# Kernel optimization log

Hardware: AMD Instinct MI355X
Metric: run time of the kernel (lower is better)

## Reference

```python
import jax, jax.numpy as jnp
import numpy as np

EPS_LN1 = 1e-6   # partial(nn.LayerNorm, eps=1e-6)
EPS_OUT = 1e-5   # nn.LayerNorm default inside SS3D out_norm


def _layernorm(x, w, b, eps):
    m = jnp.mean(x, axis=-1, keepdims=True)
    v = jnp.var(x, axis=-1, keepdims=True)
    return (x - m) * jax.lax.rsqrt(v + eps) * w + b


def _selective_scan(dA, dBx):
    # dA, dBx: (B, K, d, L, N); linear recurrence h_t = dA_t * h_{t-1} + dBx_t
    def comb(c1, c2):
        a1, b1 = c1
        a2, b2 = c2
        return a2 * a1, a2 * b1 + b2
    _, hs = jax.lax.associative_scan(comb, (dA, dBx), axis=3)
    return hs  # (B, K, d, L, N)


def setup_inputs() -> dict:
    key = jax.random.key(0)
    ks = jax.random.split(key, 12)
    B, D, H, W, C = 1, 16, 16, 16, 96
    d, N, K, R = 96, 16, 6, 6  # d_inner, d_state, n_scan_dirs, dt_rank
    s = 0.02
    f = lambda k, shp: jax.random.normal(k, shp, dtype=jnp.float32)
    return {
        "x": f(ks[0], (B, D, H, W, C)),
        "ln1_w": jnp.ones((C,), jnp.float32),
        "ln1_b": jnp.zeros((C,), jnp.float32),
        "in_proj_w": f(ks[1], (2 * d, C)) * s,
        "conv_w": f(ks[2], (d, 1, 3, 3, 3)) * s,
        "conv_b": f(ks[3], (d,)) * s,
        "x_proj_w": f(ks[4], (K, R + 2 * N, d)) * s,
        "dt_proj_w": f(ks[5], (K, d, R)) * s,
        "dt_proj_b": f(ks[6], (K, d)) * s,
        "A_log": jnp.log(1.0 + 15.0 * jax.random.uniform(ks[7], (K, d, N), jnp.float32)),
        "D_skip": f(ks[8], (K, d)) * s,
        "out_norm_w": jnp.ones((d,), jnp.float32),
        "out_norm_b": jnp.zeros((d,), jnp.float32),
        "out_proj_w": f(ks[9], (C, d)) * s,
    }


def reference(x, ln1_w, ln1_b, in_proj_w, conv_w, conv_b, x_proj_w,
              dt_proj_w, dt_proj_b, A_log, D_skip, out_norm_w, out_norm_b,
              out_proj_w):
    B, D, H, W, C = x.shape
    L = D * H * W
    K, _, d = x_proj_w.shape
    R = dt_proj_w.shape[2]
    N = A_log.shape[2]

    # pre-norm
    xn = _layernorm(x, ln1_w, ln1_b, EPS_LN1)

    # in_proj -> (x, z)
    xz = jnp.einsum('bdhwc,ec->bdhwe', xn, in_proj_w)  # (B,D,H,W,2d)
    xh, z = jnp.split(xz, 2, axis=-1)

    # depthwise 3x3x3 conv + SiLU, channels-first
    xc = jnp.transpose(xh, (0, 4, 1, 2, 3))  # (B,d,D,H,W)
    xc = jax.lax.conv_general_dilated(
        xc, conv_w, window_strides=(1, 1, 1), padding='SAME',
        dimension_numbers=('NCDHW', 'OIDHW', 'NCDHW'),
        feature_group_count=d)
    xc = jax.nn.silu(xc + conv_b[None, :, None, None, None])

    # K = 6 scan orderings: DHW, HWD, WDH and their reverses
    o0 = xc.reshape(B, d, L)
    o1 = jnp.transpose(xc, (0, 1, 3, 4, 2)).reshape(B, d, L)  # (H,W,D) order
    o2 = jnp.transpose(xc, (0, 1, 4, 2, 3)).reshape(B, d, L)  # (W,D,H) order
    fwd3 = jnp.stack([o0, o1, o2], axis=1)                    # (B,3,d,L)
    xs = jnp.concatenate([fwd3, jnp.flip(fwd3, axis=-1)], axis=1)  # (B,K,d,L)

    # per-direction input-dependent parameters
    x_dbl = jnp.einsum('bkdl,kcd->bkcl', xs, x_proj_w)        # (B,K,R+2N,L)
    dt, Bm, Cm = jnp.split(x_dbl, [R, R + N], axis=2)
    dts = jnp.einsum('bkrl,kdr->bkdl', dt, dt_proj_w) + dt_proj_b[None, :, :, None]
    dts = jax.nn.softplus(dts)                                # delta_softplus

    A = -jnp.exp(A_log)                                       # (K,d,N)
    dA = jnp.exp(dts[..., None] * A[None, :, :, None, :])     # (B,K,d,L,N)
    Bt = jnp.transpose(Bm, (0, 1, 3, 2))                      # (B,K,L,N)
    dBx = (dts * xs)[..., None] * Bt[:, :, None, :, :]        # (B,K,d,L,N)

    hs = _selective_scan(dA, dBx)                             # (B,K,d,L,N)
    Ct = jnp.transpose(Cm, (0, 1, 3, 2))                      # (B,K,L,N)
    ys = jnp.einsum('bkdln,bkln->bkdl', hs, Ct) + D_skip[None, :, :, None] * xs

    # undo reversals and orderings, sum the 6 paths
    yf = ys[:, :3] + jnp.flip(ys[:, 3:], axis=-1)             # (B,3,d,L)
    y0 = yf[:, 0]
    y1 = jnp.transpose(yf[:, 1].reshape(B, d, H, W, D), (0, 1, 4, 2, 3)).reshape(B, d, L)
    y2 = jnp.transpose(yf[:, 2].reshape(B, d, W, D, H), (0, 1, 3, 4, 2)).reshape(B, d, L)
    y = (y0 + y1 + y2).reshape(B, d, D, H, W)
    y = jnp.transpose(y, (0, 2, 3, 4, 1))                     # (B,D,H,W,d)

    # out_norm, gate, out_proj
    y = _layernorm(y, out_norm_w, out_norm_b, EPS_OUT)
    y = y * jax.nn.silu(z)
    out = jnp.einsum('bdhwe,ce->bdhwc', y, out_proj_w)

    # residual (drop_path is identity at eval)
    return x + out
```

## Files before the change

### kernel.cpp

```cpp
#include <hip/hip_runtime.h>
#include <hip/hip_bf16.h>

#define L 4096
#define CDIM 96
#define DDIM 96
#define KDIR 6
#define NST 16
#define RRK 6
#define YH 32
#define NCHUNK 256
#define CHLEN 16

typedef _Float16 half4v __attribute__((ext_vector_type(4)));

__device__ __forceinline__ float sigmoidf_(float x) { return 1.f / (1.f + __expf(-x)); }

__device__ __forceinline__ int sigma_k(int kb, int l) {
    if (kb == 0) return l;
    if (kb == 1) return ((l & 15) << 8) | ((l >> 8) << 4) | ((l >> 4) & 15);
    return (((l >> 4) & 15) << 8) | ((l & 15) << 4) | (l >> 8);
}

__global__ void __launch_bounds__(192) k1_ln_inproj(
        const float* __restrict__ x, const float* __restrict__ ln_w,
        const float* __restrict__ ln_b, const float* __restrict__ Wp,
        _Float16* __restrict__ xhh, _Float16* __restrict__ zsh) {
    int s0 = blockIdx.x * 8;
    int tid = threadIdx.x;
    __shared__ __align__(16) float xt[8][96];
    __shared__ __align__(16) float xn[8][96];
    __shared__ float mss[8], rss[8];
    ((float4*)&xt[0][0])[tid] = ((const float4*)(x + (size_t)s0 * 96))[tid];
    __syncthreads();
    int wave = tid >> 6, lane = tid & 63;
    for (int r = wave; r < 8; r += 3) {
        float v = xt[r][lane] + ((lane < 32) ? xt[r][64 + lane] : 0.f);
#pragma unroll
        for (int off = 1; off < 64; off <<= 1) v += __shfl_xor(v, off);
        float vs = xt[r][lane] * xt[r][lane] + ((lane < 32) ? xt[r][64 + lane] * xt[r][64 + lane] : 0.f);
#pragma unroll
        for (int off = 1; off < 64; off <<= 1) vs += __shfl_xor(vs, off);
        if (lane == 0) {
            float mean = v * (1.f / 96.f);
            float var = vs * (1.f / 96.f) - mean * mean;
            mss[r] = mean; rss[r] = rsqrtf(var + 1e-6f);
        }
    }
    __syncthreads();
    {
        int r = tid / 24, c4 = tid % 24;
        float4 xv = ((float4*)&xt[r][0])[c4];
        float4 wv = ((const float4*)ln_w)[c4];
        float4 bv = ((const float4*)ln_b)[c4];
        float m = mss[r], rs = rss[r];
        float4 o;
        o.x = (xv.x - m) * rs * wv.x + bv.x;
        o.y = (xv.y - m) * rs * wv.y + bv.y;
        o.z = (xv.z - m) * rs * wv.z + bv.z;
        o.w = (xv.w - m) * rs * wv.w + bv.w;
        ((float4*)&xn[r][0])[c4] = o;
    }
    float4 Wr[24];
    const float4* wr = (const float4*)(Wp + (size_t)tid * 96);
#pragma unroll
    for (int c4 = 0; c4 < 24; c4++) Wr[c4] = wr[c4];
    __syncthreads();
#pragma unroll
    for (int s = 0; s < 8; s++) {
        const float4* xr4 = (const float4*)&xn[s][0];
        float a0 = 0.f, a1 = 0.f, a2 = 0.f, a3 = 0.f;
#pragma unroll
        for (int c4 = 0; c4 < 24; c4 += 4) {
            float4 x0 = xr4[c4], x1 = xr4[c4 + 1], x2 = xr4[c4 + 2], x3 = xr4[c4 + 3];
            a0 += Wr[c4].x * x0.x + Wr[c4].y * x0.y + Wr[c4].z * x0.z + Wr[c4].w * x0.w;
            a1 += Wr[c4+1].x * x1.x + Wr[c4+1].y * x1.y + Wr[c4+1].z * x1.z + Wr[c4+1].w * x1.w;
            a2 += Wr[c4+2].x * x2.x + Wr[c4+2].y * x2.y + Wr[c4+2].z * x2.z + Wr[c4+2].w * x2.w;
            a3 += Wr[c4+3].x * x3.x + Wr[c4+3].y * x3.y + Wr[c4+3].z * x3.z + Wr[c4+3].w * x3.w;
        }
        float acc = (a0 + a1) + (a2 + a3);
        if (tid < 96) xhh[(size_t)tid * L + s0 + s] = (_Float16)acc;
        else zsh[(size_t)(s0 + s) * 96 + (tid - 96)] = (_Float16)(acc * sigmoidf_(acc));
    }
}

__global__ void k2_conv(const _Float16* __restrict__ xhh, const float* __restrict__ cw,
                        const float* __restrict__ cb, _Float16* __restrict__ xch,
                        _Float16* __restrict__ xcTh) {
    int idx = blockIdx.x * 256 + threadIdx.x;
    int c = idx >> 12, s = idx & 4095;
    int dz = s >> 8, h = (s >> 4) & 15, w = s & 15;
    const _Float16* xin = xhh + (size_t)c * L;
    const float* wc = cw + c * 27;
    float acc = cb[c];
#pragma unroll
    for (int i = 0; i < 3; i++) {
        int z2 = dz + i - 1; if ((unsigned)z2 > 15u) continue;
#pragma unroll
        for (int j = 0; j < 3; j++) {
            int h2 = h + j - 1; if ((unsigned)h2 > 15u) continue;
#pragma unroll
            for (int kk = 0; kk < 3; kk++) {
                int w2 = w + kk - 1; if ((unsigned)w2 > 15u) continue;
                acc += (float)xin[z2 * 256 + h2 * 16 + w2] * wc[i * 9 + j * 3 + kk];
            }
        }
    }
    float r = acc * sigmoidf_(acc);
    _Float16 hr = (_Float16)r;
    xch[(size_t)c * L + s] = hr;
    xcTh[(size_t)s * 96 + c] = hr;
}

__global__ void k3_xproj(const _Float16* __restrict__ xch, const float* __restrict__ Wx,
                         const float* __restrict__ Wdt, const float* __restrict__ bdt,
                         _Float16* __restrict__ Y2h, _Float16* __restrict__ Zsh) {
    int k = blockIdx.x;
    int tid = threadIdx.x;
    int sbase = blockIdx.y * 256;
    int s = sbase + tid;
    int g = blockIdx.z;
    __shared__ float dts[256][6];
    float acc[14];
#pragma unroll
    for (int i = 0; i < 14; i++) acc[i] = 0.f;
    const float* wdt_rows = Wx + (size_t)k * 38 * DDIM;
    const float* wbc      = Wx + ((size_t)k * 38 + 6 + g * 8) * DDIM;
    for (int dd = 0; dd < 96; dd += 4) {
        float v[4];
#pragma unroll
        for (int j = 0; j < 4; j++) v[j] = (float)xch[(size_t)(dd + j) * L + s];
#pragma unroll
        for (int j = 0; j < 4; j++) {
#pragma unroll
            for (int r = 0; r < 6; r++) acc[r] += wdt_rows[r * DDIM + dd + j] * v[j];
#pragma unroll
            for (int i = 0; i < 8; i++) acc[6 + i] += wbc[i * DDIM + dd + j] * v[j];
        }
    }
    _Float16* yo = Y2h + ((size_t)k * L + s) * YH;
#pragma unroll
    for (int i = 0; i < 8; i++) yo[g * 8 + i] = (_Float16)acc[6 + i];
#pragma unroll
    for (int r = 0; r < 6; r++) dts[tid][r] = acc[r];
    __syncthreads();
    for (int i = 0; i < 24; i++) {
        int idx = i * 256 + tid;
        int dl = idx % 24;
        int sr = idx / 24;
        int d = g * 24 + dl;
        const float* wr = Wdt + ((size_t)k * 96 + d) * 6;
        float a = bdt[k * 96 + d];
#pragma unroll
        for (int r = 0; r < 6; r++) a += wr[r] * dts[sr][r];
        float sp = (a > 15.f) ? a : __logf(1.f + __expf(a));
        Zsh[((size_t)k * L + sbase + sr) * 96 + d] = (_Float16)sp;
    }
}


__global__ void __launch_bounds__(256) ka_scan(
        const _Float16* __restrict__ Zsh, const _Float16* __restrict__ xcTh,
        const _Float16* __restrict__ Y2h, const float* __restrict__ A_log,
        _Float16* __restrict__ Aah, _Float16* __restrict__ Abh) {
    int t = blockIdx.x * 256 + threadIdx.x;
    int nq = t & 3;
    int q = t >> 2;
    int d = q % 96;
    int rest = q / 96;
    int chunk = rest % NCHUNK;
    int k = rest / NCHUNK;
    int kb = (k < 3) ? k : (k - 3);
    bool flip = (k >= 3);
    float An[4];
    {
        float4 al = *(const float4*)(A_log + ((size_t)k * 96 + d) * 16 + nq * 4);
        An[0] = -__expf(al.x); An[1] = -__expf(al.y);
        An[2] = -__expf(al.z); An[3] = -__expf(al.w);
    }
    float a[4] = {1.f, 1.f, 1.f, 1.f};
    float b[4] = {0.f, 0.f, 0.f, 0.f};
    const _Float16* Zk = Zsh + (size_t)k * L * 96;
    const _Float16* Yk = Y2h + (size_t)k * L * YH;
    int l0 = chunk * CHLEN;
    for (int i = 0; i < CHLEN; i += 4) {
        int sI[4]; float dt[4], xv[4]; half4v Bh[4];
#pragma unroll
        for (int j = 0; j < 4; j++) {
            int l = l0 + i + j;
            int lp = flip ? (4095 - l) : l;
            sI[j] = sigma_k(kb, lp);
        }
#pragma unroll
        for (int j = 0; j < 4; j++) {
            dt[j] = (float)Zk[(size_t)sI[j] * 96 + d];
            xv[j] = (float)xcTh[(size_t)sI[j] * 96 + d];
            Bh[j] = *(const half4v*)(Yk + (size_t)sI[j] * YH + nq * 4);
        }
#pragma unroll
        for (int j = 0; j < 4; j++) {
            float dtx = dt[j] * xv[j];
            float e0 = __expf(dt[j] * An[0]);
            float e1 = __expf(dt[j] * An[1]);
            float e2 = __expf(dt[j] * An[2]);
            float e3 = __expf(dt[j] * An[3]);
            b[0] = e0 * b[0] + dtx * (float)Bh[j].x; a[0] *= e0;
            b[1] = e1 * b[1] + dtx * (float)Bh[j].y; a[1] *= e1;
            b[2] = e2 * b[2] + dtx * (float)Bh[j].z; a[2] *= e2;
            b[3] = e3 * b[3] + dtx * (float)Bh[j].w; a[3] *= e3;
        }
    }
    size_t o = (((size_t)k * NCHUNK + chunk) * 96 + d) * 16 + nq * 4;
    half4v ha, hb;
    ha.x = (_Float16)a[0]; ha.y = (_Float16)a[1]; ha.z = (_Float16)a[2]; ha.w = (_Float16)a[3];
    hb.x = (_Float16)b[0]; hb.y = (_Float16)b[1]; hb.z = (_Float16)b[2]; hb.w = (_Float16)b[3];
    *(half4v*)(Aah + o) = ha;
    *(half4v*)(Abh + o) = hb;
}

__global__ void __launch_bounds__(256) kb_combine(
        const _Float16* __restrict__ Aah, const _Float16* __restrict__ Abh,
        _Float16* __restrict__ Pbh) {
    int t = blockIdx.x * 256 + threadIdx.x;
    int n = t & 15;
    int rest = t >> 4;
    int d = rest % 96;
    int k = rest / 96;
    size_t base = ((size_t)k * NCHUNK * 96 + d) * 16 + n;
    const size_t cstride = 96 * 16;
    float rb = 0.f;
    for (int c0 = 0; c0 < NCHUNK; c0 += 16) {
        float av[16], bv[16];
#pragma unroll
        for (int j = 0; j < 16; j++) {
            av[j] = (float)Aah[base + (size_t)(c0 + j) * cstride];
            bv[j] = (float)Abh[base + (size_t)(c0 + j) * cstride];
        }
#pragma unroll
        for (int j = 0; j < 16; j++) {
            Pbh[base + (size_t)(c0 + j) * cstride] = (_Float16)rb;
            rb = av[j] * rb + bv[j];
        }
    }
}

__global__ void __launch_bounds__(256) kc_apply(
        const _Float16* __restrict__ Zsh, const _Float16* __restrict__ xcTh,
        const _Float16* __restrict__ Y2h, const float* __restrict__ A_log,
        const float* __restrict__ D_skip, const _Float16* __restrict__ Pbh,
        _Float16* __restrict__ ysh) {
    int t = blockIdx.x * 256 + threadIdx.x;
    int nq = t & 3;
    int q = t >> 2;
    int d = q % 96;
    int rest = q / 96;
    int chunk = rest % NCHUNK;
    int k = rest / NCHUNK;
    int kb = (k < 3) ? k : (k - 3);
    bool flip = (k >= 3);
    float An[4];
    {
        float4 al = *(const float4*)(A_log + ((size_t)k * 96 + d) * 16 + nq * 4);
        An[0] = -__expf(al.x); An[1] = -__expf(al.y);
        An[2] = -__expf(al.z); An[3] = -__expf(al.w);
    }
    float Dk = D_skip[k * DDIM + d];
    float h[4];
    {
        half4v hp = *(const half4v*)(Pbh + (((size_t)k * NCHUNK + chunk) * 96 + d) * 16 + nq * 4);
        h[0] = (float)hp.x; h[1] = (float)hp.y; h[2] = (float)hp.z; h[3] = (float)hp.w;
    }
    const _Float16* Zk = Zsh + (size_t)k * L * 96;
    const _Float16* Yk = Y2h + (size_t)k * L * YH;
    int l0 = chunk * CHLEN;
    for (int i = 0; i < CHLEN; i += 4) {
        int sI[4]; float dt[4], xv[4]; half4v Bh[4], Ch[4];
#pragma unroll
        for (int j = 0; j < 4; j++) {
            int l = l0 + i + j;
            int lp = flip ? (4095 - l) : l;
            sI[j] = sigma_k(kb, lp);
        }
#pragma unroll
        for (int j = 0; j < 4; j++) {
            dt[j] = (float)Zk[(size_t)sI[j] * 96 + d];
            xv[j] = (float)xcTh[(size_t)sI[j] * 96 + d];
            Bh[j] = *(const half4v*)(Yk + (size_t)sI[j] * YH + nq * 4);
            Ch[j] = *(const half4v*)(Yk + (size_t)sI[j] * YH + 16 + nq * 4);
        }
#pragma unroll
        for (int j = 0; j < 4; j++) {
            float dtx = dt[j] * xv[j];
            float e0 = __expf(dt[j] * An[0]);
            float e1 = __expf(dt[j] * An[1]);
            float e2 = __expf(dt[j] * An[2]);
            float e3 = __expf(dt[j] * An[3]);
            h[0] = e0 * h[0] + dtx * (float)Bh[j].x;
            h[1] = e1 * h[1] + dtx * (float)Bh[j].y;
            h[2] = e2 * h[2] + dtx * (float)Bh[j].z;
            h[3] = e3 * h[3] + dtx * (float)Bh[j].w;
            float p = h[0] * (float)Ch[j].x + h[1] * (float)Ch[j].y
                    + h[2] * (float)Ch[j].z + h[3] * (float)Ch[j].w;
            p += __shfl_xor(p, 1);
            p += __shfl_xor(p, 2);
            if (nq == 0) ysh[((size_t)sI[j] * KDIR + k) * 96 + d] = (_Float16)(p + Dk * xv[j]);
        }
    }
}

__global__ void __launch_bounds__(192) k6_out(
        const _Float16* __restrict__ ysh, const _Float16* __restrict__ zsh,
        const float* __restrict__ onw, const float* __restrict__ onb,
        const float* __restrict__ Wo, const float* __restrict__ x,
        float* __restrict__ out) {
    int s0 = blockIdx.x * 8;
    int tid = threadIdx.x;
    __shared__ __align__(16) float vt[8][96];
    __shared__ __align__(16) float gt[8][96];
    __shared__ float mss[8], rss[8];
#pragma unroll
    for (int j = 0; j < 4; j++) {
        int f = tid + j * 192;
        int sr = f / 96, c = f % 96;
        const _Float16* yr = ysh + ((size_t)(s0 + sr) * KDIR) * 96 + c;
        float v = 0.f;
#pragma unroll
        for (int k = 0; k < KDIR; k++) v += (float)yr[k * 96];
        vt[sr][c] = v;
    }
    __syncthreads();
    int wave = tid >> 6, lane = tid & 63;
    for (int r = wave; r < 8; r += 3) {
        float v = vt[r][lane] + ((lane < 32) ? vt[r][64 + lane] : 0.f);
#pragma unroll
        for (int off = 1; off < 64; off <<= 1) v += __shfl_xor(v, off);
        float vs = vt[r][lane] * vt[r][lane] + ((lane < 32) ? vt[r][64 + lane] * vt[r][64 + lane] : 0.f);
#pragma unroll
        for (int off = 1; off < 64; off <<= 1) vs += __shfl_xor(vs, off);
        if (lane == 0) {
            float mean = v * (1.f / 96.f);
            float var = vs * (1.f / 96.f) - mean * mean;
            mss[r] = mean; rss[r] = rsqrtf(var + 1e-5f);
        }
    }
    __syncthreads();
#pragma unroll
    for (int j = 0; j < 4; j++) {
        int f = tid + j * 192;
        int sr = f / 96, c = f % 96;
        float g = (vt[sr][c] - mss[sr]) * rss[sr] * onw[c] + onb[c];
        gt[sr][c] = g * (float)zsh[(size_t)(s0 + sr) * 96 + c];
    }
    int e = tid % 96, sg = tid / 96;
    float4 Wr[24];
    const float4* wr = (const float4*)(Wo + (size_t)e * 96);
#pragma unroll
    for (int c4 = 0; c4 < 24; c4++) Wr[c4] = wr[c4];
    __syncthreads();
#pragma unroll
    for (int j = 0; j < 4; j++) {
        int s = sg * 4 + j;
        const float4* g4 = (const float4*)&gt[s][0];
        float a0 = 0.f, a1 = 0.f, a2 = 0.f, a3 = 0.f;
#pragma unroll
        for (int c4 = 0; c4 < 24; c4 += 4) {
            float4 x0 = g4[c4], x1 = g4[c4 + 1], x2 = g4[c4 + 2], x3 = g4[c4 + 3];
            a0 += Wr[c4].x * x0.x + Wr[c4].y * x0.y + Wr[c4].z * x0.z + Wr[c4].w * x0.w;
            a1 += Wr[c4+1].x * x1.x + Wr[c4+1].y * x1.y + Wr[c4+1].z * x1.z + Wr[c4+1].w * x1.w;
            a2 += Wr[c4+2].x * x2.x + Wr[c4+2].y * x2.y + Wr[c4+2].z * x2.z + Wr[c4+2].w * x2.w;
            a3 += Wr[c4+3].x * x3.x + Wr[c4+3].y * x3.y + Wr[c4+3].z * x3.z + Wr[c4+3].w * x3.w;
        }
        float acc = (a0 + a1) + (a2 + a3) + x[(size_t)(s0 + s) * 96 + e];
        out[(size_t)(s0 + s) * 96 + e] = acc;
    }
}

extern "C" void kernel_launch(void* const* d_in, const int* in_sizes, int n_in,
                              void* d_out, int out_size, void* d_ws, size_t ws_size,
                              hipStream_t stream) {
    const float* x        = (const float*)d_in[0];
    const float* ln1_w    = (const float*)d_in[1];
    const float* ln1_b    = (const float*)d_in[2];
    const float* in_proj  = (const float*)d_in[3];
    const float* conv_w   = (const float*)d_in[4];
    const float* conv_b   = (const float*)d_in[5];
    const float* x_proj   = (const float*)d_in[6];
    const float* dt_w     = (const float*)d_in[7];
    const float* dt_b     = (const float*)d_in[8];
    const float* A_log    = (const float*)d_in[9];
    const float* D_skip   = (const float*)d_in[10];
    const float* onw      = (const float*)d_in[11];
    const float* onb      = (const float*)d_in[12];
    const float* out_w    = (const float*)d_in[13];
    float* out = (float*)d_out;

    _Float16* xhh  = (_Float16*)d_ws;
    _Float16* zsh  = xhh + (size_t)96 * L;
    _Float16* xch  = zsh + (size_t)96 * L;
    _Float16* xcTh = xch + (size_t)96 * L;
    _Float16* Y2h  = xcTh + (size_t)96 * L;
    _Float16* Zsh  = Y2h + (size_t)KDIR * L * YH;
    _Float16* ysh  = Zsh + (size_t)KDIR * L * 96;
    _Float16* Aah  = ysh + (size_t)L * KDIR * 96;
    _Float16* Abh  = Aah + (size_t)KDIR * NCHUNK * DDIM * NST;
    _Float16* Pbh  = Abh + (size_t)KDIR * NCHUNK * DDIM * NST;

    k1_ln_inproj<<<dim3(L / 8), dim3(192), 0, stream>>>(x, ln1_w, ln1_b, in_proj, xhh, zsh);
    k2_conv<<<dim3(96 * L / 256), dim3(256), 0, stream>>>(xhh, conv_w, conv_b, xch, xcTh);
    k3_xproj<<<dim3(KDIR, 16, 4), dim3(256), 0, stream>>>(xch, x_proj, dt_w, dt_b, Y2h, Zsh);
    ka_scan<<<dim3(KDIR * NCHUNK * DDIM * 4 / 256), dim3(256), 0, stream>>>(Zsh, xcTh, Y2h, A_log, Aah, Abh);
    kb_combine<<<dim3(KDIR * DDIM * NST / 256), dim3(256), 0, stream>>>(Aah, Abh, Pbh);
    kc_apply<<<dim3(KDIR * NCHUNK * DDIM * 4 / 256), dim3(256), 0, stream>>>(Zsh, xcTh, Y2h, A_log, D_skip, Pbh, ysh);
    k6_out<<<dim3(L / 8), dim3(192), 0, stream>>>(ysh, zsh, onw, onb, out_w, x, out);
}
```

Baseline: 178.7 us.

## Fuse all seven stages into one cooperative persistent kernel with grid syncs

Replaces the seven separate kernel launches with a single cooperative kernel of 512 persistent blocks. Each stage runs as a grid-stride loop and is separated from the next by grid.sync(). The aim is to remove launch overhead and inter-kernel gaps. In exchange, some stages lose per-stage tuned block shapes: 192-thread stages now run in 256-thread blocks with threads idle. Grid barriers also add their own cost. If the cooperative launch fails, it falls back to the original launches.

After: 531.4 us. 197% more time.

```diff
diff --git a/kernel.cpp b/kernel.cpp
--- a/kernel.cpp
+++ b/kernel.cpp
@@ -1,5 +1,8 @@
 #include <hip/hip_runtime.h>
 #include <hip/hip_bf16.h>
+#include <hip/hip_cooperative_groups.h>
+
+namespace cg = cooperative_groups;
 
 #define L 4096
 #define CDIM 96
@@ -10,6 +13,7 @@
 #define YH 32
 #define NCHUNK 256
 #define CHLEN 16
+#define GRIDN 512
 
 typedef _Float16 half4v __attribute__((ext_vector_type(4)));
 
@@ -20,6 +24,374 @@
     if (kb == 1) return ((l & 15) << 8) | ((l >> 8) << 4) | ((l >> 4) & 15);
     return (((l >> 4) & 15) << 8) | ((l & 15) << 4) | (l >> 8);
 }
+
+__global__ void __launch_bounds__(256, 2) fused_vss(
+        const float* __restrict__ x, const float* __restrict__ ln1_w,
+        const float* __restrict__ ln1_b, const float* __restrict__ in_proj,
+        const float* __restrict__ conv_w, const float* __restrict__ conv_b,
+        const float* __restrict__ x_proj, const float* __restrict__ dt_w,
+        const float* __restrict__ dt_b, const float* __restrict__ A_log,
+        const float* __restrict__ D_skip, const float* __restrict__ onw,
+        const float* __restrict__ onb, const float* __restrict__ out_w,
+        float* __restrict__ out,
+        _Float16* __restrict__ xhh, _Float16* __restrict__ zsh,
+        _Float16* __restrict__ xch, _Float16* __restrict__ xcTh,
+        _Float16* __restrict__ Y2h, _Float16* __restrict__ Zsh,
+        _Float16* __restrict__ ysh, _Float16* __restrict__ Aah,
+        _Float16* __restrict__ Abh, _Float16* __restrict__ Pbh) {
+    cg::grid_group grid = cg::this_grid();
+    const int tid = threadIdx.x;
+    const int bid = blockIdx.x;
+    const int G = gridDim.x;
+
+    __shared__ __align__(16) float smA[8][96];
+    __shared__ __align__(16) float smB[8][96];
+    __shared__ float sms[8], smr[8];
+    __shared__ float dts[256][6];
+
+    for (int u = bid; u < L / 8; u += G) {
+        int s0 = u * 8;
+        if (tid < 192)
+            ((float4*)&smA[0][0])[tid] = ((const float4*)(x + (size_t)s0 * 96))[tid];
+        __syncthreads();
+        int wave = tid >> 6, lane = tid & 63;
+        for (int r = wave; r < 8; r += 4) {
+            float v = smA[r][lane] + ((lane < 32) ? smA[r][64 + lane] : 0.f);
+#pragma unroll
+            for (int off = 1; off < 64; off <<= 1) v += __shfl_xor(v, off);
+            float vs = smA[r][lane] * smA[r][lane] + ((lane < 32) ? smA[r][64 + lane] * smA[r][64 + lane] : 0.f);
+#pragma unroll
+            for (int off = 1; off < 64; off <<= 1) vs += __shfl_xor(vs, off);
+            if (lane == 0) {
+                float mean = v * (1.f / 96.f);
+                float var = vs * (1.f / 96.f) - mean * mean;
+                sms[r] = mean; smr[r] = rsqrtf(var + 1e-6f);
+            }
+        }
+        __syncthreads();
+        if (tid < 192) {
+            int r = tid / 24, c4 = tid % 24;
+            float4 xv = ((float4*)&smA[r][0])[c4];
+            float4 wv = ((const float4*)ln1_w)[c4];
+            float4 bv = ((const float4*)ln1_b)[c4];
+            float m = sms[r], rs = smr[r];
+            float4 o;
+            o.x = (xv.x - m) * rs * wv.x + bv.x;
+            o.y = (xv.y - m) * rs * wv.y + bv.y;
+            o.z = (xv.z - m) * rs * wv.z + bv.z;
+            o.w = (xv.w - m) * rs * wv.w + bv.w;
+            ((float4*)&smB[r][0])[c4] = o;
+        }
+        float4 Wr[24];
+        if (tid < 192) {
+            const float4* wr = (const float4*)(in_proj + (size_t)tid * 96);
+#pragma unroll
+            for (int c4 = 0; c4 < 24; c4++) Wr[c4] = wr[c4];
+        }
+        __syncthreads();
+        if (tid < 192) {
+#pragma unroll
+            for (int s = 0; s < 8; s++) {
+                const float4* xr4 = (const float4*)&smB[s][0];
+                float a0 = 0.f, a1 = 0.f, a2 = 0.f, a3 = 0.f;
+#pragma unroll
+                for (int c4 = 0; c4 < 24; c4 += 4) {
+                    float4 x0 = xr4[c4], x1 = xr4[c4 + 1], x2 = xr4[c4 + 2], x3 = xr4[c4 + 3];
+                    a0 += Wr[c4].x * x0.x + Wr[c4].y * x0.y + Wr[c4].z * x0.z + Wr[c4].w * x0.w;
+                    a1 += Wr[c4+1].x * x1.x + Wr[c4+1].y * x1.y + Wr[c4+1].z * x1.z + Wr[c4+1].w * x1.w;
+                    a2 += Wr[c4+2].x * x2.x + Wr[c4+2].y * x2.y + Wr[c4+2].z * x2.z + Wr[c4+2].w * x2.w;
+                    a3 += Wr[c4+3].x * x3.x + Wr[c4+3].y * x3.y + Wr[c4+3].z * x3.z + Wr[c4+3].w * x3.w;
+                }
+                float acc = (a0 + a1) + (a2 + a3);
+                if (tid < 96) xhh[(size_t)tid * L + s0 + s] = (_Float16)acc;
+                else zsh[(size_t)(s0 + s) * 96 + (tid - 96)] = (_Float16)(acc * sigmoidf_(acc));
+            }
+        }
+        __syncthreads();
+    }
+    grid.sync();
+
+    for (int u = bid; u < (96 * L) / 256; u += G) {
+        int idx = u * 256 + tid;
+        int c = idx >> 12, s = idx & 4095;
+        int dz = s >> 8, h = (s >> 4) & 15, w = s & 15;
+        const _Float16* xin = xhh + (size_t)c * L;
+        const float* wc = conv_w + c * 27;
+        float acc = conv_b[c];
+#pragma unroll
+        for (int i = 0; i < 3; i++) {
+            int z2 = dz + i - 1; if ((unsigned)z2 > 15u) continue;
+#pragma unroll
+            for (int j = 0; j < 3; j++) {
+                int h2 = h + j - 1; if ((unsigned)h2 > 15u) continue;
+#pragma unroll
+                for (int kk = 0; kk < 3; kk++) {
+                    int w2 = w + kk - 1; if ((unsigned)w2 > 15u) continue;
+                    acc += (float)xin[z2 * 256 + h2 * 16 + w2] * wc[i * 9 + j * 3 + kk];
+                }
+            }
+        }
+        float r = acc * sigmoidf_(acc);
+        _Float16 hr = (_Float16)r;
+        xch[(size_t)c * L + s] = hr;
+        xcTh[(size_t)s * 96 + c] = hr;
+    }
+    grid.sync();
+
+    for (int u = bid; u < 384; u += G) {
+        int k = u % 6;
+        int sb = (u / 6) % 16;
+        int g = u / 96;
+        int sbase = sb * 256;
+        int s = sbase + tid;
+        float acc[14];
+#pragma unroll
+        for (int i = 0; i < 14; i++) acc[i] = 0.f;
+        const float* wdt_rows = x_proj + (size_t)k * 38 * DDIM;
+        const float* wbc      = x_proj + ((size_t)k * 38 + 6 + g * 8) * DDIM;
+        for (int dd = 0; dd < 96; dd += 4) {
+            float v[4];
+#pragma unroll
+            for (int j = 0; j < 4; j++) v[j] = (float)xch[(size_t)(dd + j) * L + s];
+#pragma unroll
+            for (int j = 0; j < 4; j++) {
+#pragma unroll
+                for (int r = 0; r < 6; r++) acc[r] += wdt_rows[r * DDIM + dd + j] * v[j];
+#pragma unroll
+                for (int i = 0; i < 8; i++) acc[6 + i] += wbc[i * DDIM + dd + j] * v[j];
+            }
+        }
+        _Float16* yo = Y2h + ((size_t)k * L + s) * YH;
+#pragma unroll
+        for (int i = 0; i < 8; i++) yo[g * 8 + i] = (_Float16)acc[6 + i];
+#pragma unroll
+        for (int r = 0; r < 6; r++) dts[tid][r] = acc[r];
+        __syncthreads();
+        for (int i = 0; i < 24; i++) {
+            int idx = i * 256 + tid;
+            int dl = idx % 24;
+            int sr = idx / 24;
+            int d = g * 24 + dl;
+            const float* wr = dt_w + ((size_t)k * 96 + d) * 6;
+            float a = dt_b[k * 96 + d];
+#pragma unroll
+            for (int r = 0; r < 6; r++) a += wr[r] * dts[sr][r];
+            float sp = (a > 15.f) ? a : __logf(1.f + __expf(a));
+            Zsh[((size_t)k * L + sbase + sr) * 96 + d] = (_Float16)sp;
+        }
+        __syncthreads();
+    }
+    grid.sync();
+
+    for (int u = bid; u < KDIR * NCHUNK * DDIM * 4 / 256; u += G) {
+        int t = u * 256 + tid;
+        int nq = t & 3;
+        int q = t >> 2;
+        int d = q % 96;
+        int rest = q / 96;
+        int chunk = rest % NCHUNK;
+        int k = rest / NCHUNK;
+        int kb = (k < 3) ? k : (k - 3);
+        bool flip = (k >= 3);
+        float An[4];
+        {
+            float4 al = *(const float4*)(A_log + ((size_t)k * 96 + d) * 16 + nq * 4);
+            An[0] = -__expf(al.x); An[1] = -__expf(al.y);
+            An[2] = -__expf(al.z); An[3] = -__expf(al.w);
+        }
+        float a[4] = {1.f, 1.f, 1.f, 1.f};
+        float b[4] = {0.f, 0.f, 0.f, 0.f};
+        const _Float16* Zk = Zsh + (size_t)k * L * 96;
+        const _Float16* Yk = Y2h + (size_t)k * L * YH;
+        int l0 = chunk * CHLEN;
+        for (int i = 0; i < CHLEN; i += 4) {
+            int sI[4]; float dt[4], xv[4]; half4v Bh[4];
+#pragma unroll
+            for (int j = 0; j < 4; j++) {
+                int l = l0 + i + j;
+                int lp = flip ? (4095 - l) : l;
+                sI[j] = sigma_k(kb, lp);
+            }
+#pragma unroll
+            for (int j = 0; j < 4; j++) {
+                dt[j] = (float)Zk[(size_t)sI[j] * 96 + d];
+                xv[j] = (float)xcTh[(size_t)sI[j] * 96 + d];
+                Bh[j] = *(const half4v*)(Yk + (size_t)sI[j] * YH + nq * 4);
+            }
+#pragma unroll
+            for (int j = 0; j < 4; j++) {
+                float dtx = dt[j] * xv[j];
+                float e0 = __expf(dt[j] * An[0]);
+                float e1 = __expf(dt[j] * An[1]);
+                float e2 = __expf(dt[j] * An[2]);
+                float e3 = __expf(dt[j] * An[3]);
+                b[0] = e0 * b[0] + dtx * (float)Bh[j].x; a[0] *= e0;
+                b[1] = e1 * b[1] + dtx * (float)Bh[j].y; a[1] *= e1;
+                b[2] = e2 * b[2] + dtx * (float)Bh[j].z; a[2] *= e2;
+                b[3] = e3 * b[3] + dtx * (float)Bh[j].w; a[3] *= e3;
+            }
+        }
+        size_t o = (((size_t)k * NCHUNK + chunk) * 96 + d) * 16 + nq * 4;
+        half4v ha, hb;
+        ha.x = (_Float16)a[0]; ha.y = (_Float16)a[1]; ha.z = (_Float16)a[2]; ha.w = (_Float16)a[3];
+        hb.x = (_Float16)b[0]; hb.y = (_Float16)b[1]; hb.z = (_Float16)b[2]; hb.w = (_Float16)b[3];
+        *(half4v*)(Aah + o) = ha;
+        *(half4v*)(Abh + o) = hb;
+    }
+    grid.sync();
+
+    for (int u = bid; u < KDIR * DDIM * NST / 256; u += G) {
+        int t = u * 256 + tid;
+        int n = t & 15;
+        int rest = t >> 4;
+        int d = rest % 96;
+        int k = rest / 96;
+        size_t base = ((size_t)k * NCHUNK * 96 + d) * 16 + n;
+        const size_t cstride = 96 * 16;
+        float rb = 0.f;
+        for (int c0 = 0; c0 < NCHUNK; c0 += 16) {
+            float av[16], bv[16];
+#pragma unroll
+            for (int j = 0; j < 16; j++) {
+                av[j] = (float)Aah[base + (size_t)(c0 + j) * cstride];
+                bv[j] = (float)Abh[base + (size_t)(c0 + j) * cstride];
+            }
+#pragma unroll
+            for (int j = 0; j < 16; j++) {
+                Pbh[base + (size_t)(c0 + j) * cstride] = (_Float16)rb;
+                rb = av[j] * rb + bv[j];
+            }
+        }
+    }
+    grid.sync();
+
+    for (int u = bid; u < KDIR * NCHUNK * DDIM * 4 / 256; u += G) {
+        int t = u * 256 + tid;
+        int nq = t & 3;
+        int q = t >> 2;
+        int d = q % 96;
+        int rest = q / 96;
+        int chunk = rest % NCHUNK;
+        int k = rest / NCHUNK;
+        int kb = (k < 3) ? k : (k - 3);
+        bool flip = (k >= 3);
+        float An[4];
+        {
+            float4 al = *(const float4*)(A_log + ((size_t)k * 96 + d) * 16 + nq * 4);
+            An[0] = -__expf(al.x); An[1] = -__expf(al.y);
+            An[2] = -__expf(al.z); An[3] = -__expf(al.w);
+        }
+        float Dk = D_skip[k * DDIM + d];
+        float h[4];
+        {
+            half4v hp = *(const half4v*)(Pbh + (((size_t)k * NCHUNK + chunk) * 96 + d) * 16 + nq * 4);
+            h[0] = (float)hp.x; h[1] = (float)hp.y; h[2] = (float)hp.z; h[3] = (float)hp.w;
+        }
+        const _Float16* Zk = Zsh + (size_t)k * L * 96;
+        const _Float16* Yk = Y2h + (size_t)k * L * YH;
+        int l0 = chunk * CHLEN;
+        for (int i = 0; i < CHLEN; i += 4) {
+            int sI[4]; float dt[4], xv[4]; half4v Bh[4], Ch[4];
+#pragma unroll
+            for (int j = 0; j < 4; j++) {
+                int l = l0 + i + j;
+                int lp = flip ? (4095 - l) : l;
+                sI[j] = sigma_k(kb, lp);
+            }
+#pragma unroll
+            for (int j = 0; j < 4; j++) {
+                dt[j] = (float)Zk[(size_t)sI[j] * 96 + d];
+                xv[j] = (float)xcTh[(size_t)sI[j] * 96 + d];
+                Bh[j] = *(const half4v*)(Yk + (size_t)sI[j] * YH + nq * 4);
+                Ch[j] = *(const half4v*)(Yk + (size_t)sI[j] * YH + 16 + nq * 4);
+            }
+#pragma unroll
+            for (int j = 0; j < 4; j++) {
+                float dtx = dt[j] * xv[j];
+                float e0 = __expf(dt[j] * An[0]);
+                float e1 = __expf(dt[j] * An[1]);
+                float e2 = __expf(dt[j] * An[2]);
+                float e3 = __expf(dt[j] * An[3]);
+                h[0] = e0 * h[0] + dtx * (float)Bh[j].x;
+                h[1] = e1 * h[1] + dtx * (float)Bh[j].y;
+                h[2] = e2 * h[2] + dtx * (float)Bh[j].z;
+                h[3] = e3 * h[3] + dtx * (float)Bh[j].w;
+                float p = h[0] * (float)Ch[j].x + h[1] * (float)Ch[j].y
+                        + h[2] * (float)Ch[j].z + h[3] * (float)Ch[j].w;
+                p += __shfl_xor(p, 1);
+                p += __shfl_xor(p, 2);
+                if (nq == 0) ysh[((size_t)sI[j] * KDIR + k) * 96 + d] = (_Float16)(p + Dk * xv[j]);
+            }
+        }
+    }
+    grid.sync();
+
+    for (int u = bid; u < L / 8; u += G) {
+        int s0 = u * 8;
+#pragma unroll
+        for (int j = 0; j < 3; j++) {
+            int f = tid + j * 256;
+            int sr = f / 96, c = f % 96;
+            const _Float16* yr = ysh + ((size_t)(s0 + sr) * KDIR) * 96 + c;
+            float v = 0.f;
+#pragma unroll
+            for (int k = 0; k < KDIR; k++) v += (float)yr[k * 96];
+            smA[sr][c] = v;
+        }
+        __syncthreads();
+        int wave = tid >> 6, lane = tid & 63;
+        for (int r = wave; r < 8; r += 4) {
+            float v = smA[r][lane] + ((lane < 32) ? smA[r][64 + lane] : 0.f);
+#pragma unroll
+            for (int off = 1; off < 64; off <<= 1) v += __shfl_xor(v, off);
+            float vs = smA[r][lane] * smA[r][lane] + ((lane < 32) ? smA[r][64 + lane] * smA[r][64 + lane] : 0.f);
+#pragma unroll
+            for (int off = 1; off < 64; off <<= 1) vs += __shfl_xor(vs, off);
+            if (lane == 0) {
+                float mean = v * (1.f / 96.f);
+                float var = vs * (1.f / 96.f) - mean * mean;
+                sms[r] = mean; smr[r] = rsqrtf(var + 1e-5f);
+            }
+        }
+        __syncthreads();
+#pragma unroll
+        for (int j = 0; j < 3; j++) {
+            int f = tid + j * 256;
+            int sr = f / 96, c = f % 96;
+            float g = (smA[sr][c] - sms[sr]) * smr[sr] * onw[c] + onb[c];
+            smB[sr][c] = g * (float)zsh[(size_t)(s0 + sr) * 96 + c];
+        }
+        float4 Wr[24];
+        if (tid < 192) {
+            int e = tid % 96;
+            const float4* wr = (const float4*)(out_w + (size_t)e * 96);
+#pragma unroll
+            for (int c4 = 0; c4 < 24; c4++) Wr[c4] = wr[c4];
+        }
+        __syncthreads();
+        if (tid < 192) {
+            int e = tid % 96, sg = tid / 96;
+#pragma unroll
+            for (int j = 0; j < 4; j++) {
+                int s = sg * 4 + j;
+                const float4* g4 = (const float4*)&smB[s][0];
+                float a0 = 0.f, a1 = 0.f, a2 = 0.f, a3 = 0.f;
+#pragma unroll
+                for (int c4 = 0; c4 < 24; c4 += 4) {
+                    float4 x0 = g4[c4], x1 = g4[c4 + 1], x2 = g4[c4 + 2], x3 = g4[c4 + 3];
+                    a0 += Wr[c4].x * x0.x + Wr[c4].y * x0.y + Wr[c4].z * x0.z + Wr[c4].w * x0.w;
+                    a1 += Wr[c4+1].x * x1.x + Wr[c4+1].y * x1.y + Wr[c4+1].z * x1.z + Wr[c4+1].w * x1.w;
+                    a2 += Wr[c4+2].x * x2.x + Wr[c4+2].y * x2.y + Wr[c4+2].z * x2.z + Wr[c4+2].w * x2.w;
+                    a3 += Wr[c4+3].x * x3.x + Wr[c4+3].y * x3.y + Wr[c4+3].z * x3.z + Wr[c4+3].w * x3.w;
+                }
+                float acc = (a0 + a1) + (a2 + a3) + x[(size_t)(s0 + s) * 96 + e];
+                out[(size_t)(s0 + s) * 96 + e] = acc;
+            }
+        }
+        __syncthreads();
+    }
+}
+
 
 __global__ void __launch_bounds__(192) k1_ln_inproj(
         const float* __restrict__ x, const float* __restrict__ ln_w,
@@ -156,7 +528,6 @@
         Zsh[((size_t)k * L + sbase + sr) * 96 + d] = (_Float16)sp;
     }
 }
-
 
 __global__ void __launch_bounds__(256) ka_scan(
         const _Float16* __restrict__ Zsh, const _Float16* __restrict__ xcTh,
@@ -404,11 +775,24 @@
     _Float16* Abh  = Aah + (size_t)KDIR * NCHUNK * DDIM * NST;
     _Float16* Pbh  = Abh + (size_t)KDIR * NCHUNK * DDIM * NST;
 
-    k1_ln_inproj<<<dim3(L / 8), dim3(192), 0, stream>>>(x, ln1_w, ln1_b, in_proj, xhh, zsh);
-    k2_conv<<<dim3(96 * L / 256), dim3(256), 0, stream>>>(xhh, conv_w, conv_b, xch, xcTh);
-    k3_xproj<<<dim3(KDIR, 16, 4), dim3(256), 0, stream>>>(xch, x_proj, dt_w, dt_b, Y2h, Zsh);
-    ka_scan<<<dim3(KDIR * NCHUNK * DDIM * 4 / 256), dim3(256), 0, stream>>>(Zsh, xcTh, Y2h, A_log, Aah, Abh);
-    kb_combine<<<dim3(KDIR * DDIM * NST / 256), dim3(256), 0, stream>>>(Aah, Abh, Pbh);
-    kc_apply<<<dim3(KDIR * NCHUNK * DDIM * 4 / 256), dim3(256), 0, stream>>>(Zsh, xcTh, Y2h, A_log, D_skip, Pbh, ysh);
-    k6_out<<<dim3(L / 8), dim3(192), 0, stream>>>(ysh, zsh, onw, onb, out_w, x, out);
-}
+    void* args[] = {
+        (void*)&x, (void*)&ln1_w, (void*)&ln1_b, (void*)&in_proj,
+        (void*)&conv_w, (void*)&conv_b, (void*)&x_proj, (void*)&dt_w,
+        (void*)&dt_b, (void*)&A_log, (void*)&D_skip, (void*)&onw,
+        (void*)&onb, (void*)&out_w, (void*)&out,
+        (void*)&xhh, (void*)&zsh, (void*)&xch, (void*)&xcTh, (void*)&Y2h,
+        (void*)&Zsh, (void*)&ysh, (void*)&Aah, (void*)&Abh, (void*)&Pbh
+    };
+    hipError_t err = hipLaunchCooperativeKernel(fused_vss, dim3(GRIDN), dim3(256),
+                                                args, 0u, stream);
+    if (err != hipSuccess) {
+        (void)hipGetLastError();
+        k1_ln_inproj<<<dim3(L / 8), dim3(192), 0, stream>>>(x, ln1_w, ln1_b, in_proj, xhh, zsh);
+        k2_conv<<<dim3(96 * L / 256), dim3(256), 0, stream>>>(xhh, conv_w, conv_b, xch, xcTh);
+        k3_xproj<<<dim3(KDIR, 16, 4), dim3(256), 0, stream>>>(xch, x_proj, dt_w, dt_b, Y2h, Zsh);
+        ka_scan<<<dim3(KDIR * NCHUNK * DDIM * 4 / 256), dim3(256), 0, stream>>>(Zsh, xcTh, Y2h, A_log, Aah, Abh);
+        kb_combine<<<dim3(KDIR * DDIM * NST / 256), dim3(256), 0, stream>>>(Aah, Abh, Pbh);
+        kc_apply<<<dim3(KDIR * NCHUNK * DDIM * 4 / 256), dim3(256), 0, stream>>>(Zsh, xcTh, Y2h, A_log, D_skip, Pbh, ysh);
+        k6_out<<<dim3(L / 8), dim3(192), 0, stream>>>(ysh, zsh, onw, onb, out_w, x, out);
+    }
+}
```

## Fuse chunked selective scan into one kernel with in-LDS chunk-prefix scan

Applied to the files above, without the earlier changes.

Replaces the three-kernel chunked scan (per-chunk reduce, global sequential combine, apply) with one kernel per (direction, channel) block. Each block does 64 chunks of 64 steps, runs a Hillis-Steele prefix over chunk carries in shared memory, then applies. This drops two launches and the fp16 round-trip of chunk carries through global memory, and the exp is rewritten as exp2 with a prescaled A. In exchange the grid shrinks to 576 blocks with longer sequential per-thread loops, which may reduce latency hiding.

After: 210.2 us. +17.7%, slower.

```diff
diff --git a/kernel.cpp b/kernel.cpp
--- a/kernel.cpp
+++ b/kernel.cpp
@@ -8,8 +8,8 @@
 #define NST 16
 #define RRK 6
 #define YH 32
-#define NCHUNK 256
-#define CHLEN 16
+#define SCHUNK 64
+#define SCLEN 64
 
 typedef _Float16 half4v __attribute__((ext_vector_type(4)));
 
@@ -157,32 +157,34 @@
     }
 }
 
-
-__global__ void __launch_bounds__(256) ka_scan(
+__global__ void __launch_bounds__(256) kscan(
         const _Float16* __restrict__ Zsh, const _Float16* __restrict__ xcTh,
         const _Float16* __restrict__ Y2h, const float* __restrict__ A_log,
-        _Float16* __restrict__ Aah, _Float16* __restrict__ Abh) {
-    int t = blockIdx.x * 256 + threadIdx.x;
-    int nq = t & 3;
-    int q = t >> 2;
-    int d = q % 96;
-    int rest = q / 96;
-    int chunk = rest % NCHUNK;
-    int k = rest / NCHUNK;
+        const float* __restrict__ D_skip, _Float16* __restrict__ ysh) {
+    int blk = blockIdx.x;
+    int k = blk / 96, d = blk % 96;
+    int tid = threadIdx.x;
+    int nq = tid & 3;
+    int chunk = tid >> 2;
     int kb = (k < 3) ? k : (k - 3);
     bool flip = (k >= 3);
+
+    __shared__ float lds_a[SCHUNK][16];
+    __shared__ float lds_b[SCHUNK][16];
+
     float An[4];
     {
         float4 al = *(const float4*)(A_log + ((size_t)k * 96 + d) * 16 + nq * 4);
-        An[0] = -__expf(al.x); An[1] = -__expf(al.y);
-        An[2] = -__expf(al.z); An[3] = -__expf(al.w);
-    }
+        An[0] = -__expf(al.x) * 1.44269504f; An[1] = -__expf(al.y) * 1.44269504f;
+        An[2] = -__expf(al.z) * 1.44269504f; An[3] = -__expf(al.w) * 1.44269504f;
+    }
+    const _Float16* Zk = Zsh + (size_t)k * L * 96;
+    const _Float16* Yk = Y2h + (size_t)k * L * YH;
+    int l0 = chunk * SCLEN;
+
     float a[4] = {1.f, 1.f, 1.f, 1.f};
     float b[4] = {0.f, 0.f, 0.f, 0.f};
-    const _Float16* Zk = Zsh + (size_t)k * L * 96;
-    const _Float16* Yk = Y2h + (size_t)k * L * YH;
-    int l0 = chunk * CHLEN;
-    for (int i = 0; i < CHLEN; i += 4) {
+    for (int i = 0; i < SCLEN; i += 4) {
         int sI[4]; float dt[4], xv[4]; half4v Bh[4];
 #pragma unroll
         for (int j = 0; j < 4; j++) {
@@ -199,80 +201,53 @@
 #pragma unroll
         for (int j = 0; j < 4; j++) {
             float dtx = dt[j] * xv[j];
-            float e0 = __expf(dt[j] * An[0]);
-            float e1 = __expf(dt[j] * An[1]);
-            float e2 = __expf(dt[j] * An[2]);
-            float e3 = __expf(dt[j] * An[3]);
+            float e0 = exp2f(dt[j] * An[0]);
+            float e1 = exp2f(dt[j] * An[1]);
+            float e2 = exp2f(dt[j] * An[2]);
+            float e3 = exp2f(dt[j] * An[3]);
             b[0] = e0 * b[0] + dtx * (float)Bh[j].x; a[0] *= e0;
             b[1] = e1 * b[1] + dtx * (float)Bh[j].y; a[1] *= e1;
             b[2] = e2 * b[2] + dtx * (float)Bh[j].z; a[2] *= e2;
             b[3] = e3 * b[3] + dtx * (float)Bh[j].w; a[3] *= e3;
         }
     }
-    size_t o = (((size_t)k * NCHUNK + chunk) * 96 + d) * 16 + nq * 4;
-    half4v ha, hb;
-    ha.x = (_Float16)a[0]; ha.y = (_Float16)a[1]; ha.z = (_Float16)a[2]; ha.w = (_Float16)a[3];
-    hb.x = (_Float16)b[0]; hb.y = (_Float16)b[1]; hb.z = (_Float16)b[2]; hb.w = (_Float16)b[3];
-    *(half4v*)(Aah + o) = ha;
-    *(half4v*)(Abh + o) = hb;
-}
-
-__global__ void __launch_bounds__(256) kb_combine(
-        const _Float16* __restrict__ Aah, const _Float16* __restrict__ Abh,
-        _Float16* __restrict__ Pbh) {
-    int t = blockIdx.x * 256 + threadIdx.x;
-    int n = t & 15;
-    int rest = t >> 4;
-    int d = rest % 96;
-    int k = rest / 96;
-    size_t base = ((size_t)k * NCHUNK * 96 + d) * 16 + n;
-    const size_t cstride = 96 * 16;
-    float rb = 0.f;
-    for (int c0 = 0; c0 < NCHUNK; c0 += 16) {
-        float av[16], bv[16];
-#pragma unroll
-        for (int j = 0; j < 16; j++) {
-            av[j] = (float)Aah[base + (size_t)(c0 + j) * cstride];
-            bv[j] = (float)Abh[base + (size_t)(c0 + j) * cstride];
-        }
-#pragma unroll
-        for (int j = 0; j < 16; j++) {
-            Pbh[base + (size_t)(c0 + j) * cstride] = (_Float16)rb;
-            rb = av[j] * rb + bv[j];
-        }
-    }
-}
-
-__global__ void __launch_bounds__(256) kc_apply(
-        const _Float16* __restrict__ Zsh, const _Float16* __restrict__ xcTh,
-        const _Float16* __restrict__ Y2h, const float* __restrict__ A_log,
-        const float* __restrict__ D_skip, const _Float16* __restrict__ Pbh,
-        _Float16* __restrict__ ysh) {
-    int t = blockIdx.x * 256 + threadIdx.x;
-    int nq = t & 3;
-    int q = t >> 2;
-    int d = q % 96;
-    int rest = q / 96;
-    int chunk = rest % NCHUNK;
-    int k = rest / NCHUNK;
-    int kb = (k < 3) ? k : (k - 3);
-    bool flip = (k >= 3);
-    float An[4];
-    {
-        float4 al = *(const float4*)(A_log + ((size_t)k * 96 + d) * 16 + nq * 4);
-        An[0] = -__expf(al.x); An[1] = -__expf(al.y);
-        An[2] = -__expf(al.z); An[3] = -__expf(al.w);
-    }
+#pragma unroll
+    for (int i = 0; i < 4; i++) {
+        lds_a[chunk][nq * 4 + i] = a[i];
+        lds_b[chunk][nq * 4 + i] = b[i];
+    }
+    __syncthreads();
+
+    for (int off = 1; off < SCHUNK; off <<= 1) {
+        float na[4], nb[4]; int cc[4], st[4]; bool act[4];
+#pragma unroll
+        for (int j = 0; j < 4; j++) {
+            int idx = tid + j * 256;
+            int c = idx >> 4, s2 = idx & 15;
+            cc[j] = c; st[j] = s2;
+            act[j] = (c >= off);
+            if (act[j]) {
+                float pa = lds_a[c - off][s2], pb = lds_b[c - off][s2];
+                float ca = lds_a[c][s2],       cb = lds_b[c][s2];
+                na[j] = ca * pa;
+                nb[j] = ca * pb + cb;
+            }
+        }
+        __syncthreads();
+#pragma unroll
+        for (int j = 0; j < 4; j++) {
+            if (act[j]) { lds_a[cc[j]][st[j]] = na[j]; lds_b[cc[j]][st[j]] = nb[j]; }
+        }
+        __syncthreads();
+    }
+
+    float h[4];
+#pragma unroll
+    for (int i = 0; i < 4; i++)
+        h[i] = (chunk == 0) ? 0.f : lds_b[chunk - 1][nq * 4 + i];
     float Dk = D_skip[k * DDIM + d];
-    float h[4];
-    {
-        half4v hp = *(const half4v*)(Pbh + (((size_t)k * NCHUNK + chunk) * 96 + d) * 16 + nq * 4);
-        h[0] = (float)hp.x; h[1] = (float)hp.y; h[2] = (float)hp.z; h[3] = (float)hp.w;
-    }
-    const _Float16* Zk = Zsh + (size_t)k * L * 96;
-    const _Float16* Yk = Y2h + (size_t)k * L * YH;
-    int l0 = chunk * CHLEN;
-    for (int i = 0; i < CHLEN; i += 4) {
+
+    for (int i = 0; i < SCLEN; i += 4) {
         int sI[4]; float dt[4], xv[4]; half4v Bh[4], Ch[4];
 #pragma unroll
         for (int j = 0; j < 4; j++) {
@@ -290,10 +265,10 @@
 #pragma unroll
         for (int j = 0; j < 4; j++) {
             float dtx = dt[j] * xv[j];
-            float e0 = __expf(dt[j] * An[0]);
-            float e1 = __expf(dt[j] * An[1]);
-            float e2 = __expf(dt[j] * An[2]);
-            float e3 = __expf(dt[j] * An[3]);
+            float e0 = exp2f(dt[j] * An[0]);
+            float e1 = exp2f(dt[j] * An[1]);
+            float e2 = exp2f(dt[j] * An[2]);
+            float e3 = exp2f(dt[j] * An[3]);
             h[0] = e0 * h[0] + dtx * (float)Bh[j].x;
             h[1] = e1 * h[1] + dtx * (float)Bh[j].y;
             h[2] = e2 * h[2] + dtx * (float)Bh[j].z;
@@ -400,15 +375,10 @@
     _Float16* Y2h  = xcTh + (size_t)96 * L;
     _Float16* Zsh  = Y2h + (size_t)KDIR * L * YH;
     _Float16* ysh  = Zsh + (size_t)KDIR * L * 96;
-    _Float16* Aah  = ysh + (size_t)L * KDIR * 96;
-    _Float16* Abh  = Aah + (size_t)KDIR * NCHUNK * DDIM * NST;
-    _Float16* Pbh  = Abh + (size_t)KDIR * NCHUNK * DDIM * NST;
 
     k1_ln_inproj<<<dim3(L / 8), dim3(192), 0, stream>>>(x, ln1_w, ln1_b, in_proj, xhh, zsh);
     k2_conv<<<dim3(96 * L / 256), dim3(256), 0, stream>>>(xhh, conv_w, conv_b, xch, xcTh);
     k3_xproj<<<dim3(KDIR, 16, 4), dim3(256), 0, stream>>>(xch, x_proj, dt_w, dt_b, Y2h, Zsh);
-    ka_scan<<<dim3(KDIR * NCHUNK * DDIM * 4 / 256), dim3(256), 0, stream>>>(Zsh, xcTh, Y2h, A_log, Aah, Abh);
-    kb_combine<<<dim3(KDIR * DDIM * NST / 256), dim3(256), 0, stream>>>(Aah, Abh, Pbh);
-    kc_apply<<<dim3(KDIR * NCHUNK * DDIM * 4 / 256), dim3(256), 0, stream>>>(Zsh, xcTh, Y2h, A_log, D_skip, Pbh, ysh);
+    kscan<<<dim3(KDIR * DDIM), dim3(256), 0, stream>>>(Zsh, xcTh, Y2h, A_log, D_skip, ysh);
     k6_out<<<dim3(L / 8), dim3(192), 0, stream>>>(ysh, zsh, onw, onb, out_w, x, out);
 }
```
